# Performance work log

Measured on AMD Instinct MI355X. Metric: run time of the kernel, lower is better.

Reference implementation:

```python
import jax, jax.numpy as jnp
import numpy as np

E = 131072   # total messages
N = 8192     # dim_size (num nodes)
D = 256      # input_dim == hidden_dim (forced by h + m add)


def setup_inputs() -> dict:
    key = jax.random.key(0)
    k1, k2, k3, k4, k5 = jax.random.split(key, 5)
    msg = jax.random.normal(k1, (E, D), dtype=jnp.float32)
    index = jax.random.randint(k2, (E,), 0, N)
    t = jax.random.uniform(k3, (E,), dtype=jnp.float32)
    # torch.nn.Linear(D, D) params (kaiming-uniform-ish scale)
    W = jax.random.normal(k4, (D, D), dtype=jnp.float32) / np.sqrt(D)
    b = (jax.random.normal(k5, (D,), dtype=jnp.float32) * 0.01)
    return {"msg": msg, "index": index, "t": t, "dim_size": N, "W": W, "b": b}


def reference(msg, index, t, dim_size, W, b):
    # Original: for each node, sort its messages by t, then run the linear
    # recurrence h <- W @ (m + h) + b starting from h = 0; nodes with no
    # messages keep h = 0. Vectorized: one global stable sort by (index, t),
    # then a single segmented lax.scan with reset at segment boundaries.
    num_msgs, d = msg.shape
    order = jnp.lexsort((t, index))          # primary key: index, secondary: t
    m_sorted = msg[order]                     # [E, d]
    seg = index[order]                        # [E]

    def step(carry, inp):
        h, prev = carry
        m, s = inp
        h_in = jnp.where(s == prev, h, jnp.zeros_like(h))  # reset at new segment
        h_new = (m + h_in) @ W.T + b
        return (h_new, s), h_new

    init = (jnp.zeros((d,), msg.dtype), jnp.asarray(-1, seg.dtype))
    _, ys = jax.lax.scan(step, init, (m_sorted, seg))      # ys: [E, d]

    # final hidden per node = h at the last message of its segment
    pos = jnp.arange(num_msgs)
    last = jax.ops.segment_max(pos, seg, num_segments=dim_size)
    counts = jax.ops.segment_sum(jnp.ones((num_msgs,), jnp.int32), seg,
                                 num_segments=dim_size)
    gathered = ys[jnp.clip(last, 0, num_msgs - 1)]          # [N, d]
    hidden = jnp.where((counts > 0)[:, None], gathered, jnp.zeros_like(gathered))
    return hidden
```

## Files before the change

### kernel.cpp

```cpp
#include <hip/hip_runtime.h>
#include <hip/hip_bf16.h>

#define E_MSGS 131072
#define N_NODES 8192
#define D_DIM 256
#define XA_STRIDE 280
#define SMAX 64

typedef __bf16 bf16x8 __attribute__((ext_vector_type(8)));
typedef float f32x4 __attribute__((ext_vector_type(4)));

#define BAR() asm volatile("s_waitcnt lgkmcnt(0)\n\ts_barrier" ::: "memory")


__global__ void k_count(const int* __restrict__ index, int* __restrict__ counts) {
    int e = blockIdx.x * blockDim.x + threadIdx.x;
    if (e < E_MSGS) atomicAdd(&counts[index[e]], 1);
}

__global__ void k_prep(const int* __restrict__ counts, int* __restrict__ offsets,
                       int* __restrict__ perm) {
    __shared__ int partial[1024];
    __shared__ int hist[256];
    __shared__ int hcur[256];
    int tid = threadIdx.x;
    if (tid < 256) hist[tid] = 0;
    __syncthreads();

    int base = tid * 8;
    int4 c0 = ((const int4*)counts)[tid * 2];
    int4 c1 = ((const int4*)counts)[tid * 2 + 1];
    int cs[8] = {c0.x, c0.y, c0.z, c0.w, c1.x, c1.y, c1.z, c1.w};
    int local[8];
    int sum = 0;
#pragma unroll
    for (int i = 0; i < 8; i++) {
        local[i] = sum;
        sum += cs[i];
        atomicAdd(&hist[min(cs[i], 255)], 1);
    }
    partial[tid] = sum;
    __syncthreads();
    for (int off = 1; off < 1024; off <<= 1) {
        int v = (tid >= off) ? partial[tid - off] : 0;
        __syncthreads();
        partial[tid] += v;
        __syncthreads();
    }
    int basesum = (tid > 0) ? partial[tid - 1] : 0;
#pragma unroll
    for (int i = 0; i < 8; i++) offsets[base + i] = basesum + local[i];
    if (tid == 1023) offsets[N_NODES] = partial[1023];
    __syncthreads();

    if (tid < 256) partial[tid] = hist[255 - tid];
    __syncthreads();
    for (int off = 1; off < 256; off <<= 1) {
        int v = (tid < 256 && tid >= off) ? partial[tid - off] : 0;
        __syncthreads();
        if (tid < 256) partial[tid] += v;
        __syncthreads();
    }
    if (tid < 256) hcur[tid] = partial[255 - tid] - hist[tid];
    __syncthreads();
#pragma unroll
    for (int i = 0; i < 8; i++) {
        int c = min(cs[i], 255);
        int pos = atomicAdd(&hcur[c], 1);
        perm[pos] = base + i;
    }
}

__global__ void k_scatter(const int* __restrict__ index, const int* __restrict__ offsets,
                          int* __restrict__ cursors, int* __restrict__ bucket) {
    int e = blockIdx.x * blockDim.x + threadIdx.x;
    if (e < E_MSGS) {
        int n = index[e];
        int p = offsets[n] + atomicAdd(&cursors[n], 1);
        bucket[p] = e;
    }
}

__global__ void k_sortseg(const float* __restrict__ t, const int* __restrict__ offsets,
                          const int* __restrict__ bucket, int* __restrict__ sorted_id) {
    int wid = (blockIdx.x * 256 + threadIdx.x) >> 6;
    int ln = threadIdx.x & 63;
    int beg = offsets[wid], end = offsets[wid + 1];
    int cnt = end - beg;
    int e = 0; float tv = 0.f;
    if (ln < cnt) { e = bucket[beg + ln]; tv = t[e]; }
    int rank = 0;
    for (int j = 0; j < cnt; j++) {
        float tj = __shfl(tv, j);
        int ej = __shfl(e, j);
        rank += (tj < tv) || (tj == tv && ej < e);
    }
    if (ln < cnt) sorted_id[beg + rank] = e;
}


__launch_bounds__(256, 2)
__global__ void k_gru(const float* __restrict__ msg, const float* __restrict__ W,
                      const float* __restrict__ b, const int* __restrict__ offsets,
                      const int* __restrict__ sorted_id, const int* __restrict__ perm,
                      float* __restrict__ out) {
    __shared__ __bf16 xA[2][16 * XA_STRIDE];
    __shared__ int sidT[16][SMAX];

    int tid  = threadIdx.x;
    int wave = tid >> 6;
    int lane = tid & 63;
    int q    = lane >> 4;
    int l    = lane & 15;
    int node0 = blockIdx.x * 16;

    bf16x8 wf[8][4];
#pragma unroll
    for (int t4 = 0; t4 < 4; t4++) {
        const float* wr = W + (64 * wave + 16 * t4 + l) * D_DIM;
#pragma unroll
        for (int c = 0; c < 8; c++) {
            int k0 = 32 * c + 8 * q;
            float4 w0 = *(const float4*)(wr + k0);
            float4 w1 = *(const float4*)(wr + k0 + 4);
            bf16x8 f;
            f[0] = (__bf16)w0.x; f[1] = (__bf16)w0.y; f[2] = (__bf16)w0.z; f[3] = (__bf16)w0.w;
            f[4] = (__bf16)w1.x; f[5] = (__bf16)w1.y; f[6] = (__bf16)w1.z; f[7] = (__bf16)w1.w;
            wf[c][t4] = f;
        }
    }
    float bias[4];
#pragma unroll
    for (int t4 = 0; t4 < 4; t4++) bias[t4] = b[64 * wave + 16 * t4 + l];

    int nodeC[4], cnt4[4];
#pragma unroll
    for (int r = 0; r < 4; r++) {
        int n = perm[node0 + 4 * q + r];
        nodeC[r] = n;
        cnt4[r] = offsets[n + 1] - offsets[n];
    }
    int nfirst = perm[node0];
    int S = min(offsets[nfirst + 1] - offsets[nfirst], SMAX);

    {
        int i = tid >> 4;
        int ni = perm[node0 + i];
        int o0 = offsets[ni];
        int cn = offsets[ni + 1] - o0;
#pragma unroll
        for (int j = tid & 15; j < SMAX; j += 16)
            sidT[i][j] = (cn > 0) ? sorted_id[o0 + min(j, cn - 1)] : 0;
    }
    BAR();

    float h[4][4];
#pragma unroll
    for (int t4 = 0; t4 < 4; t4++)
#pragma unroll
        for (int r = 0; r < 4; r++) h[t4][r] = 0.f;

    float mvA[4][4], mvB[4][4], mvC[4][4];
#pragma unroll
    for (int r = 0; r < 4; r++) {
        const float* m0 = msg + (long)sidT[4 * q + r][0] * D_DIM;
#pragma unroll
        for (int t4 = 0; t4 < 4; t4++)
            xA[0][(4 * q + r) * XA_STRIDE + 64 * wave + 16 * t4 + l] =
                (__bf16)m0[64 * wave + 16 * t4 + l];
    }
#pragma unroll
    for (int r = 0; r < 4; r++) {
        const float* m1 = msg + (long)sidT[4 * q + r][1] * D_DIM;
#pragma unroll
        for (int t4 = 0; t4 < 4; t4++) mvA[r][t4] = m1[64 * wave + 16 * t4 + l];
    }
#pragma unroll
    for (int r = 0; r < 4; r++) {
        const float* m2 = msg + (long)sidT[4 * q + r][2] * D_DIM;
#pragma unroll
        for (int t4 = 0; t4 < 4; t4++) mvB[r][t4] = m2[64 * wave + 16 * t4 + l];
    }
    BAR();

    auto step = [&](int s, float (&cur)[4][4], float (&nxt)[4][4]) {
        int slot = min(s + 3, SMAX - 1);
#pragma unroll
        for (int r = 0; r < 4; r++) {
            const float* mrow = msg + (long)sidT[4 * q + r][slot] * D_DIM;
#pragma unroll
            for (int t4 = 0; t4 < 4; t4++) nxt[r][t4] = mrow[64 * wave + 16 * t4 + l];
        }

        const __bf16* buf = xA[s & 1];
        f32x4 acc[4];
#pragma unroll
        for (int t4 = 0; t4 < 4; t4++) acc[t4] = (f32x4){0.f, 0.f, 0.f, 0.f};
#pragma unroll
        for (int c = 0; c < 8; c++) {
            bf16x8 a = *(const bf16x8*)(buf + l * XA_STRIDE + 32 * c + 8 * q);
#pragma unroll
            for (int t4 = 0; t4 < 4; t4++)
                acc[t4] = __builtin_amdgcn_mfma_f32_16x16x32_bf16(a, wf[c][t4], acc[t4], 0, 0, 0);
        }

        __bf16* nbuf = xA[(s + 1) & 1];
#pragma unroll
        for (int t4 = 0; t4 < 4; t4++) {
#pragma unroll
            for (int r = 0; r < 4; r++) {
                float hn = acc[t4][r] + bias[t4];
                bool valid = s < cnt4[r];
                h[t4][r] = valid ? hn : h[t4][r];
                nbuf[(4 * q + r) * XA_STRIDE + 64 * wave + 16 * t4 + l] =
                    (__bf16)(h[t4][r] + cur[r][t4]);
            }
        }
        BAR();
    };

    int s = 0;
    while (s < S) {
        step(s, mvA, mvC); s++;
        if (s >= S) break;
        step(s, mvB, mvA); s++;
        if (s >= S) break;
        step(s, mvC, mvB); s++;
    }

#pragma unroll
    for (int t4 = 0; t4 < 4; t4++)
#pragma unroll
        for (int r = 0; r < 4; r++)
            out[(long)nodeC[r] * D_DIM + 64 * wave + 16 * t4 + l] = h[t4][r];
}


extern "C" void kernel_launch(void* const* d_in, const int* in_sizes, int n_in,
                              void* d_out, int out_size, void* d_ws, size_t ws_size,
                              hipStream_t stream) {
    const float* msg   = (const float*)d_in[0];
    const int*   index = (const int*)d_in[1];
    const float* t     = (const float*)d_in[2];
    const float* W     = (const float*)d_in[4];
    const float* b     = (const float*)d_in[5];
    float* out = (float*)d_out;

    int* ws = (int*)d_ws;
    int* counts    = ws;
    int* cursors   = ws + 8192;
    int* offsets   = ws + 16384;
    int* perm      = ws + 24584;
    int* bucket    = ws + 32776;
    int* sorted_id = ws + 163848;

    hipMemsetAsync(counts, 0, 16384 * sizeof(int), stream);

    k_count<<<E_MSGS / 256, 256, 0, stream>>>(index, counts);
    k_prep<<<1, 1024, 0, stream>>>(counts, offsets, perm);
    k_scatter<<<E_MSGS / 256, 256, 0, stream>>>(index, offsets, cursors, bucket);
    k_sortseg<<<N_NODES * 64 / 256, 256, 0, stream>>>(t, offsets, bucket, sorted_id);
    k_gru<<<N_NODES / 16, 256, 0, stream>>>(msg, W, b, offsets, sorted_id, perm, out);
}
```

Baseline: 267.7 us.

## Split GRU output columns across eight waves per block instead of four

The recurrence kernel now launches 512 threads per block, so each wave owns 32 output columns instead of 64. This halves per-wave weight fragments, MFMAs and accumulators on the serial per-step critical path. The message prefetch depth drops from three to two steps to save registers, bias is folded into the accumulator init, and the LDS row stride is shrunk. The trade-off is more waves contending at each barrier and less latency hiding for the gathered message loads.

```diff
diff --git a/kernel.cpp b/kernel.cpp
--- a/kernel.cpp
+++ b/kernel.cpp
@@ -4,7 +4,7 @@
 #define E_MSGS 131072
 #define N_NODES 8192
 #define D_DIM 256
-#define XA_STRIDE 280
+#define XA_STRIDE 264
 #define SMAX 64
 
 typedef __bf16 bf16x8 __attribute__((ext_vector_type(8)));
@@ -99,7 +99,7 @@
 }
 
 
-__launch_bounds__(256, 2)
+__launch_bounds__(512, 4)
 __global__ void k_gru(const float* __restrict__ msg, const float* __restrict__ W,
                       const float* __restrict__ b, const int* __restrict__ offsets,
                       const int* __restrict__ sorted_id, const int* __restrict__ perm,
@@ -114,10 +114,10 @@
     int l    = lane & 15;
     int node0 = blockIdx.x * 16;
 
-    bf16x8 wf[8][4];
-#pragma unroll
-    for (int t4 = 0; t4 < 4; t4++) {
-        const float* wr = W + (64 * wave + 16 * t4 + l) * D_DIM;
+    bf16x8 wf[8][2];
+#pragma unroll
+    for (int t2 = 0; t2 < 2; t2++) {
+        const float* wr = W + (32 * wave + 16 * t2 + l) * D_DIM;
 #pragma unroll
         for (int c = 0; c < 8; c++) {
             int k0 = 32 * c + 8 * q;
@@ -126,12 +126,12 @@
             bf16x8 f;
             f[0] = (__bf16)w0.x; f[1] = (__bf16)w0.y; f[2] = (__bf16)w0.z; f[3] = (__bf16)w0.w;
             f[4] = (__bf16)w1.x; f[5] = (__bf16)w1.y; f[6] = (__bf16)w1.z; f[7] = (__bf16)w1.w;
-            wf[c][t4] = f;
-        }
-    }
-    float bias[4];
-#pragma unroll
-    for (int t4 = 0; t4 < 4; t4++) bias[t4] = b[64 * wave + 16 * t4 + l];
+            wf[c][t2] = f;
+        }
+    }
+    float bias[2];
+#pragma unroll
+    for (int t2 = 0; t2 < 2; t2++) bias[t2] = b[32 * wave + 16 * t2 + l];
 
     int nodeC[4], cnt4[4];
 #pragma unroll
@@ -144,76 +144,69 @@
     int S = min(offsets[nfirst + 1] - offsets[nfirst], SMAX);
 
     {
-        int i = tid >> 4;
+        int i = tid >> 5;
         int ni = perm[node0 + i];
         int o0 = offsets[ni];
         int cn = offsets[ni + 1] - o0;
 #pragma unroll
-        for (int j = tid & 15; j < SMAX; j += 16)
+        for (int j = tid & 31; j < SMAX; j += 32)
             sidT[i][j] = (cn > 0) ? sorted_id[o0 + min(j, cn - 1)] : 0;
     }
     BAR();
 
-    float h[4][4];
-#pragma unroll
-    for (int t4 = 0; t4 < 4; t4++)
-#pragma unroll
-        for (int r = 0; r < 4; r++) h[t4][r] = 0.f;
-
-    float mvA[4][4], mvB[4][4], mvC[4][4];
+    float h[2][4];
+#pragma unroll
+    for (int t2 = 0; t2 < 2; t2++)
+#pragma unroll
+        for (int r = 0; r < 4; r++) h[t2][r] = 0.f;
+
+    float mvA[4][2], mvB[4][2];
 #pragma unroll
     for (int r = 0; r < 4; r++) {
         const float* m0 = msg + (long)sidT[4 * q + r][0] * D_DIM;
 #pragma unroll
-        for (int t4 = 0; t4 < 4; t4++)
-            xA[0][(4 * q + r) * XA_STRIDE + 64 * wave + 16 * t4 + l] =
-                (__bf16)m0[64 * wave + 16 * t4 + l];
+        for (int t2 = 0; t2 < 2; t2++)
+            xA[0][(4 * q + r) * XA_STRIDE + 32 * wave + 16 * t2 + l] =
+                (__bf16)m0[32 * wave + 16 * t2 + l];
     }
 #pragma unroll
     for (int r = 0; r < 4; r++) {
         const float* m1 = msg + (long)sidT[4 * q + r][1] * D_DIM;
 #pragma unroll
-        for (int t4 = 0; t4 < 4; t4++) mvA[r][t4] = m1[64 * wave + 16 * t4 + l];
-    }
-#pragma unroll
-    for (int r = 0; r < 4; r++) {
-        const float* m2 = msg + (long)sidT[4 * q + r][2] * D_DIM;
-#pragma unroll
-        for (int t4 = 0; t4 < 4; t4++) mvB[r][t4] = m2[64 * wave + 16 * t4 + l];
+        for (int t2 = 0; t2 < 2; t2++) mvA[r][t2] = m1[32 * wave + 16 * t2 + l];
     }
     BAR();
 
-    auto step = [&](int s, float (&cur)[4][4], float (&nxt)[4][4]) {
-        int slot = min(s + 3, SMAX - 1);
+    auto step = [&](int s, float (&cur)[4][2], float (&nxt)[4][2]) {
+        int slot = min(s + 2, SMAX - 1);
 #pragma unroll
         for (int r = 0; r < 4; r++) {
             const float* mrow = msg + (long)sidT[4 * q + r][slot] * D_DIM;
 #pragma unroll
-            for (int t4 = 0; t4 < 4; t4++) nxt[r][t4] = mrow[64 * wave + 16 * t4 + l];
+            for (int t2 = 0; t2 < 2; t2++) nxt[r][t2] = mrow[32 * wave + 16 * t2 + l];
         }
 
         const __bf16* buf = xA[s & 1];
-        f32x4 acc[4];
-#pragma unroll
-        for (int t4 = 0; t4 < 4; t4++) acc[t4] = (f32x4){0.f, 0.f, 0.f, 0.f};
+        f32x4 acc[2];
+#pragma unroll
+        for (int t2 = 0; t2 < 2; t2++)
+            acc[t2] = (f32x4){bias[t2], bias[t2], bias[t2], bias[t2]};
 #pragma unroll
         for (int c = 0; c < 8; c++) {
             bf16x8 a = *(const bf16x8*)(buf + l * XA_STRIDE + 32 * c + 8 * q);
-#pragma unroll
-            for (int t4 = 0; t4 < 4; t4++)
-                acc[t4] = __builtin_amdgcn_mfma_f32_16x16x32_bf16(a, wf[c][t4], acc[t4], 0, 0, 0);
+            acc[0] = __builtin_amdgcn_mfma_f32_16x16x32_bf16(a, wf[c][0], acc[0], 0, 0, 0);
+            acc[1] = __builtin_amdgcn_mfma_f32_16x16x32_bf16(a, wf[c][1], acc[1], 0, 0, 0);
         }
 
         __bf16* nbuf = xA[(s + 1) & 1];
 #pragma unroll
-        for (int t4 = 0; t4 < 4; t4++) {
-#pragma unroll
-            for (int r = 0; r < 4; r++) {
-                float hn = acc[t4][r] + bias[t4];
-                bool valid = s < cnt4[r];
-                h[t4][r] = valid ? hn : h[t4][r];
-                nbuf[(4 * q + r) * XA_STRIDE + 64 * wave + 16 * t4 + l] =
-                    (__bf16)(h[t4][r] + cur[r][t4]);
+        for (int r = 0; r < 4; r++) {
+            bool valid = s < cnt4[r];
+#pragma unroll
+            for (int t2 = 0; t2 < 2; t2++) {
+                h[t2][r] = valid ? acc[t2][r] : h[t2][r];
+                nbuf[(4 * q + r) * XA_STRIDE + 32 * wave + 16 * t2 + l] =
+                    (__bf16)(h[t2][r] + cur[r][t2]);
             }
         }
         BAR();
@@ -221,18 +214,16 @@
 
     int s = 0;
     while (s < S) {
-        step(s, mvA, mvC); s++;
+        step(s, mvA, mvB); s++;
         if (s >= S) break;
         step(s, mvB, mvA); s++;
-        if (s >= S) break;
-        step(s, mvC, mvB); s++;
-    }
-
-#pragma unroll
-    for (int t4 = 0; t4 < 4; t4++)
+    }
+
+#pragma unroll
+    for (int t2 = 0; t2 < 2; t2++)
 #pragma unroll
         for (int r = 0; r < 4; r++)
-            out[(long)nodeC[r] * D_DIM + 64 * wave + 16 * t4 + l] = h[t4][r];
+            out[(long)nodeC[r] * D_DIM + 32 * wave + 16 * t2 + l] = h[t2][r];
 }
 
 
@@ -260,5 +251,5 @@
     k_prep<<<1, 1024, 0, stream>>>(counts, offsets, perm);
     k_scatter<<<E_MSGS / 256, 256, 0, stream>>>(index, offsets, cursors, bucket);
     k_sortseg<<<N_NODES * 64 / 256, 256, 0, stream>>>(t, offsets, bucket, sorted_id);
-    k_gru<<<N_NODES / 16, 256, 0, stream>>>(msg, W, b, offsets, sorted_id, perm, out);
-}
+    k_gru<<<N_NODES / 16, 512, 0, stream>>>(msg, W, b, offsets, sorted_id, perm, out);
+}
```

Measured after the change: 268.4 us. About the same (+0.3%).
